# Kernel tuning notes

Measured on AMD Instinct MI355X. Metric: run time of the kernel, lower is better.

Reference implementation:

```python
import jax, jax.numpy as jnp
import numpy as np
import math

D_MODEL = 1024
NHEAD = 16
D_K = D_MODEL // NHEAD
NUM_LAYERS = 4
D_FF = 4096
SEQ = 2048
BATCH = 1
EPS = 1e-5


def _layer_norm(x, g, b):
    mu = jnp.mean(x, axis=-1, keepdims=True)
    var = jnp.mean((x - mu) ** 2, axis=-1, keepdims=True)
    return (x - mu) * jax.lax.rsqrt(var + EPS) * g + b


def setup_inputs() -> dict:
    key = jax.random.key(0)
    ks = jax.random.split(key, 16)
    s = 0.02
    L, D, F = NUM_LAYERS, D_MODEL, D_FF
    inp = {
        "x": jax.random.normal(ks[0], (BATCH, SEQ, D), dtype=jnp.float32),
        "wq": jax.random.normal(ks[1], (L, D, D), dtype=jnp.float32) * s,
        "bq": jnp.zeros((L, D), dtype=jnp.float32),
        "wk": jax.random.normal(ks[2], (L, D, D), dtype=jnp.float32) * s,
        "bk": jnp.zeros((L, D), dtype=jnp.float32),
        "wv": jax.random.normal(ks[3], (L, D, D), dtype=jnp.float32) * s,
        "bv": jnp.zeros((L, D), dtype=jnp.float32),
        "wo": jax.random.normal(ks[4], (L, D, D), dtype=jnp.float32) * s,
        "bo": jnp.zeros((L, D), dtype=jnp.float32),
        "w1": jax.random.normal(ks[5], (L, D, F), dtype=jnp.float32) * s,
        "b1": jnp.zeros((L, F), dtype=jnp.float32),
        "w2": jax.random.normal(ks[6], (L, F, D), dtype=jnp.float32) * s,
        "b2": jnp.zeros((L, D), dtype=jnp.float32),
        "ln1_g": jnp.ones((L, D), dtype=jnp.float32),
        "ln1_b": jnp.zeros((L, D), dtype=jnp.float32),
        "ln2_g": jnp.ones((L, D), dtype=jnp.float32),
        "ln2_b": jnp.zeros((L, D), dtype=jnp.float32),
    }
    return inp


def _transformer(x, wq, bq, wk, bk, wv, bv, wo, bo, w1, b1, w2, b2,
                 ln1_g, ln1_b, ln2_g, ln2_b):
    B, S, D = x.shape
    scale = math.sqrt(D_K)
    for l in range(NUM_LAYERS):
        # multi-head self-attention (manual QKV matmul + softmax + matmul)
        q = (x @ wq[l] + bq[l]).reshape(B, S, NHEAD, D_K).transpose(0, 2, 1, 3)
        k = (x @ wk[l] + bk[l]).reshape(B, S, NHEAD, D_K).transpose(0, 2, 1, 3)
        v = (x @ wv[l] + bv[l]).reshape(B, S, NHEAD, D_K).transpose(0, 2, 1, 3)
        scores = jnp.einsum('bhqd,bhkd->bhqk', q, k) / scale  # [B,H,S,S]
        attn = jax.nn.softmax(scores, axis=-1)
        ctx = jnp.einsum('bhqk,bhkd->bhqd', attn, v)
        ctx = ctx.transpose(0, 2, 1, 3).reshape(B, S, D)
        attn_out = ctx @ wo[l] + bo[l]
        x = _layer_norm(x + attn_out, ln1_g[l], ln1_b[l])
        # feed-forward network with gelu
        h = jax.nn.gelu(x @ w1[l] + b1[l])
        ffn_out = h @ w2[l] + b2[l]
        x = _layer_norm(x + ffn_out, ln2_g[l], ln2_b[l])
    return x


def reference(x, wq, bq, wk, bk, wv, bv, wo, bo, w1, b1, w2, b2,
              ln1_g, ln1_b, ln2_g, ln2_b):
    return _transformer(x, wq, bq, wk, bk, wv, bv, wo, bo, w1, b1, w2, b2,
                        ln1_g, ln1_b, ln2_g, ln2_b)
```

## Files before the change

### kernel.cpp

```cpp
#include <hip/hip_runtime.h>
#include <hip/hip_bf16.h>
#include <math.h>

typedef __hip_bfloat16 bf16;
typedef __attribute__((ext_vector_type(8))) short bf16x8;
typedef __attribute__((ext_vector_type(4))) short bf16x4;
typedef __attribute__((ext_vector_type(4))) float f32x4;

#define EPI_NONE 0
#define EPI_BIAS_BF16 1
#define EPI_BIAS_GELU_BF16 2

#define CLOG 0.18033688f

__device__ __forceinline__ void gload16(const void* g, void* l) {
  __builtin_amdgcn_global_load_lds((const __attribute__((address_space(1))) void*)g,
                                   (__attribute__((address_space(3))) void*)l, 16, 0, 0);
}

__device__ __forceinline__ float gelu_tanh(float x) {
  const float c = 0.7978845608028654f;
  float t = tanhf(c * (x + 0.044715f * x * x * x));
  return 0.5f * x * (1.0f + t);
}

__device__ __forceinline__ short bf16bits(float x) {
  bf16 h = __float2bfloat16(x);
  return *reinterpret_cast<const short*>(&h);
}

template<int BM, int BN, int BK, int EPI, typename CT>
__global__ __launch_bounds__(256) void gemm_bt(
    const bf16* __restrict__ A, long sAz, int lda,
    const bf16* __restrict__ Bt, long sBz, int ldb,
    CT* __restrict__ C, long sCz, int ldc,
    const float* __restrict__ bias,
    int K, float scale)
{
  constexpr int WM = BM / 2, WN = BN / 2;
  constexpr int MI = WM / 16, NJ = WN / 16;
  constexpr int NA = (BM * BK * 2) / 4096;
  constexpr int NB = (BN * BK * 2) / 4096;
  constexpr int ROWB = BK * 2;
  __shared__ __align__(16) bf16 As[BM * BK];
  __shared__ __align__(16) bf16 Bs[BN * BK];
  const int t = threadIdx.x;
  const int lane = t & 63, w = t >> 6;
  const int wm = (w >> 1) * WM, wn = (w & 1) * WN;
  const int quad = lane >> 4, r16 = lane & 15;
  const long z = blockIdx.z;
  const bf16* Ab = A + z * sAz + (long)blockIdx.y * BM * lda;
  const bf16* Bb = Bt + z * sBz + (long)blockIdx.x * BN * ldb;

  f32x4 acc[MI][NJ];
  #pragma unroll
  for (int i = 0; i < MI; ++i)
    #pragma unroll
    for (int j = 0; j < NJ; ++j)
      acc[i][j] = (f32x4){0.f, 0.f, 0.f, 0.f};

  for (int k0 = 0; k0 < K; k0 += BK) {
    __syncthreads();
    #pragma unroll
    for (int s = 0; s < NA; ++s) {
      int Lb = s * 4096 + t * 16;
      int row = Lb / ROWB, colb = Lb % ROWB;
      gload16((const char*)Ab + (long)row * (lda * 2) + k0 * 2 + colb, (char*)As + Lb);
    }
    #pragma unroll
    for (int s = 0; s < NB; ++s) {
      int Lb = s * 4096 + t * 16;
      int row = Lb / ROWB, colb = Lb % ROWB;
      gload16((const char*)Bb + (long)row * (ldb * 2) + k0 * 2 + colb, (char*)Bs + Lb);
    }
    __syncthreads();

    #pragma unroll
    for (int kk = 0; kk < BK / 32; ++kk) {
      bf16x8 af[MI], bfv[NJ];
      #pragma unroll
      for (int i = 0; i < MI; ++i)
        af[i] = *(const bf16x8*)&As[(wm + i * 16 + r16) * BK + kk * 32 + quad * 8];
      #pragma unroll
      for (int j = 0; j < NJ; ++j)
        bfv[j] = *(const bf16x8*)&Bs[(wn + j * 16 + r16) * BK + kk * 32 + quad * 8];
      #pragma unroll
      for (int i = 0; i < MI; ++i)
        #pragma unroll
        for (int j = 0; j < NJ; ++j)
          acc[i][j] = __builtin_amdgcn_mfma_f32_16x16x32_bf16(af[i], bfv[j], acc[i][j], 0, 0, 0);
    }
  }

  CT* Cb = C + z * sCz;
  #pragma unroll
  for (int i = 0; i < MI; ++i) {
    #pragma unroll
    for (int j = 0; j < NJ; ++j) {
      int col = blockIdx.x * BN + wn + j * 16 + r16;
      float bvv = 0.f;
      if constexpr (EPI == EPI_BIAS_BF16 || EPI == EPI_BIAS_GELU_BF16)
        bvv = bias[col];
      #pragma unroll
      for (int r = 0; r < 4; ++r) {
        long row = (long)blockIdx.y * BM + wm + i * 16 + quad * 4 + r;
        float val = acc[i][j][r] * scale + bvv;
        if constexpr (EPI == EPI_BIAS_GELU_BF16) val = gelu_tanh(val);
        if constexpr (sizeof(CT) == 2)
          Cb[row * (long)ldc + col] = __float2bfloat16(val);
        else
          Cb[row * (long)ldc + col] = val;
      }
    }
  }
}

__global__ __launch_bounds__(256) void flash_attn(
    const bf16* __restrict__ qkv, const bf16* __restrict__ vT,
    float* __restrict__ Osp, float2* __restrict__ ml)
{
  constexpr int SEQ = 2048, LDP = 72, LDPP = 80;
  __shared__ __align__(16) bf16 Qs[64 * 64];
  __shared__ __align__(16) bf16 Ks[64 * LDP];
  __shared__ __align__(16) bf16 VTs[64 * LDP];
  __shared__ __align__(16) bf16 Ps[64 * LDPP];

  const int t = threadIdx.x;
  const int lane = t & 63, w = t >> 6;
  const int quad = lane >> 4, r16 = lane & 15;
  const int wq0 = w * 16;
  const int s0 = blockIdx.x * 64;
  const int h = blockIdx.y;
  const int split = blockIdx.z;
  const int kt0 = split * 16, ktN = kt0 + 16;

  #pragma unroll
  for (int s = 0; s < 2; ++s) {
    int Lb = s * 4096 + t * 16;
    int row = Lb >> 7, colb = Lb & 127;
    int4 v = *(const int4*)(qkv + (long)(s0 + row) * 3072 + h * 64 + (colb >> 1));
    *(int4*)((char*)Qs + Lb) = v;
  }

  const bf16* kp[2]; const bf16* vp[2];
  int krow[2], kcolb[2];
  #pragma unroll
  for (int s = 0; s < 2; ++s) {
    int Lb = s * 4096 + t * 16;
    krow[s] = Lb >> 7; kcolb[s] = Lb & 127;
    kp[s] = qkv + 1024 + (long)h * 64 + (long)krow[s] * 3072 + (kcolb[s] >> 1);
    vp[s] = vT + (long)(h * 64 + krow[s]) * SEQ + (kcolb[s] >> 1);
  }

  int4 rk[2], rv[2];
  #pragma unroll
  for (int s = 0; s < 2; ++s) {
    rk[s] = *(const int4*)(kp[s] + (long)kt0 * 64 * 3072);
    rv[s] = *(const int4*)(vp[s] + (long)kt0 * 64);
  }

  __syncthreads();
  bf16x8 af_q[2];
  #pragma unroll
  for (int kk = 0; kk < 2; ++kk)
    af_q[kk] = *(const bf16x8*)&Qs[(wq0 + r16) * 64 + kk * 32 + quad * 8];

  f32x4 O[4];
  float m_s = -1e30f, l_s = 0.f;
  #pragma unroll
  for (int jd = 0; jd < 4; ++jd) O[jd] = (f32x4){0.f, 0.f, 0.f, 0.f};

  for (int kt = kt0; kt < ktN; ++kt) {
    __syncthreads();
    #pragma unroll
    for (int s = 0; s < 2; ++s) {
      *(int4*)((char*)Ks + (krow[s] * LDP * 2) + kcolb[s]) = rk[s];
      *(int4*)((char*)VTs + (krow[s] * LDP * 2) + kcolb[s]) = rv[s];
    }
    __syncthreads();

    if (kt + 1 < ktN) {
      long k0n = (long)(kt + 1) * 64;
      #pragma unroll
      for (int s = 0; s < 2; ++s) {
        rk[s] = *(const int4*)(kp[s] + k0n * 3072);
        rv[s] = *(const int4*)(vp[s] + k0n);
      }
    }

    f32x4 sc[4];
    #pragma unroll
    for (int j = 0; j < 4; ++j) sc[j] = (f32x4){0.f, 0.f, 0.f, 0.f};
    #pragma unroll
    for (int kk = 0; kk < 2; ++kk) {
      bf16x8 bk_f[4];
      #pragma unroll
      for (int j = 0; j < 4; ++j)
        bk_f[j] = *(const bf16x8*)&Ks[(j * 16 + r16) * LDP + kk * 32 + quad * 8];
      #pragma unroll
      for (int j = 0; j < 4; ++j)
        sc[j] = __builtin_amdgcn_mfma_f32_16x16x32_bf16(bk_f[j], af_q[kk], sc[j], 0, 0, 0);
    }

    float mj[4];
    #pragma unroll
    for (int j = 0; j < 4; ++j)
      mj[j] = fmaxf(fmaxf(sc[j][0], sc[j][1]), fmaxf(sc[j][2], sc[j][3]));
    float mx = fmaxf(fmaxf(mj[0], mj[1]), fmaxf(mj[2], mj[3]));
    mx = fmaxf(mx, __shfl_xor(mx, 16));
    mx = fmaxf(mx, __shfl_xor(mx, 32));
    float m_new = fmaxf(m_s, mx * CLOG);
    float alpha = exp2f(m_s - m_new);
    m_s = m_new;
    float p[4][4], sj[4];
    #pragma unroll
    for (int j = 0; j < 4; ++j) {
      #pragma unroll
      for (int r = 0; r < 4; ++r)
        p[j][r] = exp2f(fmaf(sc[j][r], CLOG, -m_new));
      sj[j] = (p[j][0] + p[j][1]) + (p[j][2] + p[j][3]);
    }
    float rs = (sj[0] + sj[1]) + (sj[2] + sj[3]);
    rs += __shfl_xor(rs, 16);
    rs += __shfl_xor(rs, 32);
    l_s = l_s * alpha + rs;

    float ar[4];
    #pragma unroll
    for (int r = 0; r < 4; ++r)
      ar[r] = __shfl(alpha, quad * 20 + r);
    #pragma unroll
    for (int jd = 0; jd < 4; ++jd)
      #pragma unroll
      for (int r = 0; r < 4; ++r)
        O[jd][r] *= ar[r];

    {
      bf16* pr = &Ps[(wq0 + r16) * LDPP + quad * 4];
      #pragma unroll
      for (int j = 0; j < 4; ++j) {
        bf16x4 pk;
        #pragma unroll
        for (int r = 0; r < 4; ++r)
          pk[r] = bf16bits(p[j][r]);
        *(bf16x4*)(pr + j * 16) = pk;
      }
    }

    #pragma unroll
    for (int kk = 0; kk < 2; ++kk) {
      bf16x8 af_p, bv_f[4];
      af_p = *(const bf16x8*)&Ps[(wq0 + r16) * LDPP + kk * 32 + quad * 8];
      #pragma unroll
      for (int jd = 0; jd < 4; ++jd)
        bv_f[jd] = *(const bf16x8*)&VTs[(jd * 16 + r16) * LDP + kk * 32 + quad * 8];
      #pragma unroll
      for (int jd = 0; jd < 4; ++jd)
        O[jd] = __builtin_amdgcn_mfma_f32_16x16x32_bf16(af_p, bv_f[jd], O[jd], 0, 0, 0);
    }
  }

  float* Ob = Osp + (long)split * SEQ * 1024;
  #pragma unroll
  for (int r = 0; r < 4; ++r) {
    long row = s0 + wq0 + quad * 4 + r;
    #pragma unroll
    for (int jd = 0; jd < 4; ++jd)
      Ob[row * 1024 + h * 64 + jd * 16 + r16] = O[jd][r];
  }
  if (quad == 0)
    ml[((long)(split * 16 + h)) * SEQ + (s0 + wq0 + r16)] = make_float2(m_s, l_s);
}

__global__ __launch_bounds__(256) void attn_combine(
    const float* __restrict__ Osp, const float2* __restrict__ ml,
    bf16* __restrict__ ctx)
{
  constexpr long SD = 2048L * 1024L;
  const int s = blockIdx.x;
  const int t = threadIdx.x;
  #pragma unroll
  for (int i = 0; i < 4; ++i) {
    int c = t + i * 256;
    int h = c >> 6;
    float2 a = ml[(long)h * 2048 + s];
    float2 b = ml[(long)(16 + h) * 2048 + s];
    float mC = fmaxf(a.x, b.x);
    float w0 = exp2f(a.x - mC), w1 = exp2f(b.x - mC);
    float inv = 1.f / (a.y * w0 + b.y * w1);
    float o = (Osp[(long)s * 1024 + c] * w0 + Osp[SD + (long)s * 1024 + c] * w1) * inv;
    ctx[(long)s * 1024 + c] = __float2bfloat16(o);
  }
}

__global__ __launch_bounds__(256) void transpose_cast(
    const float* __restrict__ in, bf16* __restrict__ out, int R, int C)
{
  __shared__ bf16 tile[32][33];
  const int tx = threadIdx.x, ty = threadIdx.y;
  const int r0 = blockIdx.y * 32, c0 = blockIdx.x * 32;
  #pragma unroll
  for (int d = 0; d < 32; d += 8)
    tile[ty + d][tx] = __float2bfloat16(in[(long)(r0 + ty + d) * C + c0 + tx]);
  __syncthreads();
  #pragma unroll
  for (int d = 0; d < 32; d += 8)
    out[(long)(c0 + ty + d) * R + r0 + tx] = tile[tx][ty + d];
}

__global__ __launch_bounds__(256) void transpose_cast3(
    const float* __restrict__ w0, const float* __restrict__ w1p,
    const float* __restrict__ w2p, bf16* __restrict__ out, int R, int C)
{
  __shared__ bf16 tile[32][33];
  const float* in = (blockIdx.z == 0) ? w0 : (blockIdx.z == 1) ? w1p : w2p;
  bf16* o = out + (long)blockIdx.z * R * C;
  const int tx = threadIdx.x, ty = threadIdx.y;
  const int r0 = blockIdx.y * 32, c0 = blockIdx.x * 32;
  #pragma unroll
  for (int d = 0; d < 32; d += 8)
    tile[ty + d][tx] = __float2bfloat16(in[(long)(r0 + ty + d) * C + c0 + tx]);
  __syncthreads();
  #pragma unroll
  for (int d = 0; d < 32; d += 8)
    o[(long)(c0 + ty + d) * R + r0 + tx] = tile[tx][ty + d];
}

__global__ __launch_bounds__(256) void transpose_bf16(
    const bf16* __restrict__ in, bf16* __restrict__ out, int R, int C, int ldin)
{
  __shared__ bf16 tile[32][33];
  const int tx = threadIdx.x, ty = threadIdx.y;
  const int r0 = blockIdx.y * 32, c0 = blockIdx.x * 32;
  #pragma unroll
  for (int d = 0; d < 32; d += 8)
    tile[ty + d][tx] = in[(long)(r0 + ty + d) * ldin + c0 + tx];
  __syncthreads();
  #pragma unroll
  for (int d = 0; d < 32; d += 8)
    out[(long)(c0 + ty + d) * R + r0 + tx] = tile[tx][ty + d];
}

__device__ __forceinline__ float blk_sum(float v, float* sh) {
  #pragma unroll
  for (int o = 32; o > 0; o >>= 1) v += __shfl_down(v, o);
  __syncthreads();
  if ((threadIdx.x & 63) == 0) sh[threadIdx.x >> 6] = v;
  __syncthreads();
  return sh[0] + sh[1] + sh[2] + sh[3];
}

__global__ __launch_bounds__(256) void ln_residual2(
    float* __restrict__ X, const float* __restrict__ d0, const float* __restrict__ d1,
    const float* __restrict__ bias,
    const float* __restrict__ g, const float* __restrict__ b,
    bf16* __restrict__ xb)
{
  __shared__ float sh[4];
  const int t = threadIdx.x;
  const long base = (long)blockIdx.x * 1024;
  float v[4]; float s = 0.f;
  #pragma unroll
  for (int i = 0; i < 4; ++i) {
    int c = t + i * 256;
    float val = X[base + c] + d0[base + c] + d1[base + c] + bias[c];
    v[i] = val; s += val;
  }
  s = blk_sum(s, sh);
  const float mu = s * (1.f / 1024.f);
  float s2 = 0.f;
  #pragma unroll
  for (int i = 0; i < 4; ++i) { float d = v[i] - mu; s2 += d * d; }
  s2 = blk_sum(s2, sh);
  const float rs = rsqrtf(s2 * (1.f / 1024.f) + 1e-5f);
  #pragma unroll
  for (int i = 0; i < 4; ++i) {
    int c = t + i * 256;
    float o = (v[i] - mu) * rs * g[c] + b[c];
    X[base + c] = o;
    xb[base + c] = __float2bfloat16(o);
  }
}

__global__ __launch_bounds__(256) void init_x(
    const float* __restrict__ xin, float* __restrict__ X, bf16* __restrict__ xb, int n)
{
  for (int i = blockIdx.x * 256 + threadIdx.x; i < n; i += gridDim.x * 256) {
    float v = xin[i];
    X[i] = v;
    xb[i] = __float2bfloat16(v);
  }
}

__global__ __launch_bounds__(256) void copy_out(
    const float* __restrict__ X, float* __restrict__ out, int n)
{
  for (int i = blockIdx.x * 256 + threadIdx.x; i < n; i += gridDim.x * 256)
    out[i] = X[i];
}

__global__ __launch_bounds__(256) void concat_bias(
    const float* __restrict__ bq, const float* __restrict__ bk,
    const float* __restrict__ bv, float* __restrict__ out, int n)
{
  for (int i = blockIdx.x * 256 + threadIdx.x; i < n; i += gridDim.x * 256) {
    int l = i / 3072, r = i % 3072;
    int j = r / 1024, c = r % 1024;
    const float* src = (j == 0) ? bq : (j == 1) ? bk : bv;
    out[i] = src[l * 1024 + c];
  }
}

extern "C" void kernel_launch(void* const* d_in, const int* in_sizes, int n_in,
                              void* d_out, int out_size, void* d_ws, size_t ws_size,
                              hipStream_t stream) {
  constexpr int S = 2048, D = 1024, F = 4096, L = 4;
  const float* xin = (const float*)d_in[0];
  const float* wq = (const float*)d_in[1];
  const float* bq = (const float*)d_in[2];
  const float* wk = (const float*)d_in[3];
  const float* bk = (const float*)d_in[4];
  const float* wv = (const float*)d_in[5];
  const float* bvp = (const float*)d_in[6];
  const float* wo = (const float*)d_in[7];
  const float* bo = (const float*)d_in[8];
  const float* w1 = (const float*)d_in[9];
  const float* b1 = (const float*)d_in[10];
  const float* w2 = (const float*)d_in[11];
  const float* b2 = (const float*)d_in[12];
  const float* ln1g = (const float*)d_in[13];
  const float* ln1b = (const float*)d_in[14];
  const float* ln2g = (const float*)d_in[15];
  const float* ln2b = (const float*)d_in[16];

  char* p = (char*)d_ws;
  float* X    = (float*)p; p += (long)S * D * 4;
  float* tmpf = (float*)p; p += 2L * S * D * 4;
  bf16* xb    = (bf16*)p;  p += (long)S * D * 2;
  bf16* qkv   = (bf16*)p;
  bf16* hb    = (bf16*)p;  p += (long)S * 3 * D * 2;
  bf16* ctx   = (bf16*)p;  p += (long)S * D * 2;
  bf16* vT    = (bf16*)p;  p += (long)S * D * 2;
  bf16* wT    = (bf16*)p;  p += (long)F * D * 2;
  float* bias3= (float*)p; p += (long)L * 3 * D * 4;
  float2* ml  = (float2*)p; p += 2L * 16 * S * 8;

  init_x<<<2048, 256, 0, stream>>>(xin, X, xb, S * D);
  concat_bias<<<48, 256, 0, stream>>>(bq, bk, bvp, bias3, L * 3 * D);

  for (int l = 0; l < L; ++l) {
    transpose_cast3<<<dim3(D / 32, D / 32, 3), dim3(32, 8), 0, stream>>>(
        wq + (long)l * D * D, wk + (long)l * D * D, wv + (long)l * D * D, wT, D, D);
    gemm_bt<128, 64, 64, EPI_BIAS_BF16, bf16><<<dim3(3 * D / 64, S / 128, 1), 256, 0, stream>>>(
        xb, 0L, D, wT, 0L, D, qkv, 0L, 3 * D, bias3 + l * 3 * D, D, 1.f);

    transpose_bf16<<<dim3(D / 32, S / 32), dim3(32, 8), 0, stream>>>(qkv + 2 * D, vT, S, D, 3 * D);

    flash_attn<<<dim3(S / 64, 16, 2), 256, 0, stream>>>(qkv, vT, tmpf, ml);
    attn_combine<<<S, 256, 0, stream>>>(tmpf, ml, ctx);

    transpose_cast<<<dim3(D / 32, D / 32), dim3(32, 8), 0, stream>>>(wo + (long)l * D * D, wT, D, D);
    gemm_bt<128, 64, 64, EPI_NONE, float><<<dim3(D / 64, S / 128, 2), 256, 0, stream>>>(
        ctx, (long)(D / 2), D, wT, (long)(D / 2), D, tmpf, (long)S * D, D, nullptr, D / 2, 1.f);
    ln_residual2<<<S, 256, 0, stream>>>(X, tmpf, tmpf + (long)S * D, bo + l * D,
                                        ln1g + l * D, ln1b + l * D, xb);

    transpose_cast<<<dim3(F / 32, D / 32), dim3(32, 8), 0, stream>>>(w1 + (long)l * D * F, wT, D, F);
    gemm_bt<128, 64, 64, EPI_BIAS_GELU_BF16, bf16><<<dim3(F / 64, S / 128, 1), 256, 0, stream>>>(
        xb, 0L, D, wT, 0L, D, hb, 0L, F, b1 + l * F, D, 1.f);
    transpose_cast<<<dim3(D / 32, F / 32), dim3(32, 8), 0, stream>>>(w2 + (long)l * F * D, wT, F, D);
    gemm_bt<128, 64, 64, EPI_NONE, float><<<dim3(D / 64, S / 128, 2), 256, 0, stream>>>(
        hb, (long)(F / 2), F, wT, (long)(F / 2), F, tmpf, (long)S * D, D, nullptr, F / 2, 1.f);
    ln_residual2<<<S, 256, 0, stream>>>(X, tmpf, tmpf + (long)S * D, b2 + l * D,
                                        ln2g + l * D, ln2b + l * D, xb);
  }
  copy_out<<<2048, 256, 0, stream>>>(X, (float*)d_out, S * D);
}
```

Baseline: 1.135 ms.

## Parameterize attention split count, load Q directly, widen FFN1 GEMM tile

```diff
diff --git a/kernel.cpp b/kernel.cpp
--- a/kernel.cpp
+++ b/kernel.cpp
@@ -117,10 +117,9 @@
 
 __global__ __launch_bounds__(256) void flash_attn(
     const bf16* __restrict__ qkv, const bf16* __restrict__ vT,
-    float* __restrict__ Osp, float2* __restrict__ ml)
+    float* __restrict__ Osp, float2* __restrict__ ml, int kts)
 {
   constexpr int SEQ = 2048, LDP = 72, LDPP = 80;
-  __shared__ __align__(16) bf16 Qs[64 * 64];
   __shared__ __align__(16) bf16 Ks[64 * LDP];
   __shared__ __align__(16) bf16 VTs[64 * LDP];
   __shared__ __align__(16) bf16 Ps[64 * LDPP];
@@ -132,14 +131,13 @@
   const int s0 = blockIdx.x * 64;
   const int h = blockIdx.y;
   const int split = blockIdx.z;
-  const int kt0 = split * 16, ktN = kt0 + 16;
-
-  #pragma unroll
-  for (int s = 0; s < 2; ++s) {
-    int Lb = s * 4096 + t * 16;
-    int row = Lb >> 7, colb = Lb & 127;
-    int4 v = *(const int4*)(qkv + (long)(s0 + row) * 3072 + h * 64 + (colb >> 1));
-    *(int4*)((char*)Qs + Lb) = v;
+  const int kt0 = split * kts, ktN = kt0 + kts;
+
+  bf16x8 af_q[2];
+  {
+    const bf16* qp = qkv + (long)(s0 + wq0 + r16) * 3072 + h * 64 + quad * 8;
+    af_q[0] = *(const bf16x8*)(qp);
+    af_q[1] = *(const bf16x8*)(qp + 32);
   }
 
   const bf16* kp[2]; const bf16* vp[2];
@@ -158,12 +156,6 @@
     rk[s] = *(const int4*)(kp[s] + (long)kt0 * 64 * 3072);
     rv[s] = *(const int4*)(vp[s] + (long)kt0 * 64);
   }
-
-  __syncthreads();
-  bf16x8 af_q[2];
-  #pragma unroll
-  for (int kk = 0; kk < 2; ++kk)
-    af_q[kk] = *(const bf16x8*)&Qs[(wq0 + r16) * 64 + kk * 32 + quad * 8];
 
   f32x4 O[4];
   float m_s = -1e30f, l_s = 0.f;
@@ -274,7 +266,7 @@
 
 __global__ __launch_bounds__(256) void attn_combine(
     const float* __restrict__ Osp, const float2* __restrict__ ml,
-    bf16* __restrict__ ctx)
+    bf16* __restrict__ ctx, int nsplit)
 {
   constexpr long SD = 2048L * 1024L;
   const int s = blockIdx.x;
@@ -283,13 +275,17 @@
   for (int i = 0; i < 4; ++i) {
     int c = t + i * 256;
     int h = c >> 6;
-    float2 a = ml[(long)h * 2048 + s];
-    float2 b = ml[(long)(16 + h) * 2048 + s];
-    float mC = fmaxf(a.x, b.x);
-    float w0 = exp2f(a.x - mC), w1 = exp2f(b.x - mC);
-    float inv = 1.f / (a.y * w0 + b.y * w1);
-    float o = (Osp[(long)s * 1024 + c] * w0 + Osp[SD + (long)s * 1024 + c] * w1) * inv;
-    ctx[(long)s * 1024 + c] = __float2bfloat16(o);
+    float mC = -1e30f;
+    for (int sp = 0; sp < nsplit; ++sp)
+      mC = fmaxf(mC, ml[(long)(sp * 16 + h) * 2048 + s].x);
+    float denom = 0.f, num = 0.f;
+    for (int sp = 0; sp < nsplit; ++sp) {
+      float2 a = ml[(long)(sp * 16 + h) * 2048 + s];
+      float wv = exp2f(a.x - mC);
+      denom += a.y * wv;
+      num += Osp[sp * SD + (long)s * 1024 + c] * wv;
+    }
+    ctx[(long)s * 1024 + c] = __float2bfloat16(num / denom);
   }
 }
 
@@ -433,9 +429,12 @@
   const float* ln2g = (const float*)d_in[15];
   const float* ln2b = (const float*)d_in[16];
 
+  const int nsplit = (ws_size >= 78u * 1024 * 1024) ? 4 : 2;
+  const int kts = 32 / nsplit;
+
   char* p = (char*)d_ws;
   float* X    = (float*)p; p += (long)S * D * 4;
-  float* tmpf = (float*)p; p += 2L * S * D * 4;
+  float* tmpf = (float*)p; p += (long)nsplit * S * D * 4;
   bf16* xb    = (bf16*)p;  p += (long)S * D * 2;
   bf16* qkv   = (bf16*)p;
   bf16* hb    = (bf16*)p;  p += (long)S * 3 * D * 2;
@@ -443,7 +442,7 @@
   bf16* vT    = (bf16*)p;  p += (long)S * D * 2;
   bf16* wT    = (bf16*)p;  p += (long)F * D * 2;
   float* bias3= (float*)p; p += (long)L * 3 * D * 4;
-  float2* ml  = (float2*)p; p += 2L * 16 * S * 8;
+  float2* ml  = (float2*)p; p += (long)nsplit * 16 * S * 8;
 
   init_x<<<2048, 256, 0, stream>>>(xin, X, xb, S * D);
   concat_bias<<<48, 256, 0, stream>>>(bq, bk, bvp, bias3, L * 3 * D);
@@ -456,8 +455,8 @@
 
     transpose_bf16<<<dim3(D / 32, S / 32), dim3(32, 8), 0, stream>>>(qkv + 2 * D, vT, S, D, 3 * D);
 
-    flash_attn<<<dim3(S / 64, 16, 2), 256, 0, stream>>>(qkv, vT, tmpf, ml);
-    attn_combine<<<S, 256, 0, stream>>>(tmpf, ml, ctx);
+    flash_attn<<<dim3(S / 64, 16, nsplit), 256, 0, stream>>>(qkv, vT, tmpf, ml, kts);
+    attn_combine<<<S, 256, 0, stream>>>(tmpf, ml, ctx, nsplit);
 
     transpose_cast<<<dim3(D / 32, D / 32), dim3(32, 8), 0, stream>>>(wo + (long)l * D * D, wT, D, D);
     gemm_bt<128, 64, 64, EPI_NONE, float><<<dim3(D / 64, S / 128, 2), 256, 0, stream>>>(
@@ -466,7 +465,7 @@
                                         ln1g + l * D, ln1b + l * D, xb);
 
     transpose_cast<<<dim3(F / 32, D / 32), dim3(32, 8), 0, stream>>>(w1 + (long)l * D * F, wT, D, F);
-    gemm_bt<128, 64, 64, EPI_BIAS_GELU_BF16, bf16><<<dim3(F / 64, S / 128, 1), 256, 0, stream>>>(
+    gemm_bt<128, 128, 64, EPI_BIAS_GELU_BF16, bf16><<<dim3(F / 128, S / 128, 1), 256, 0, stream>>>(
         xb, 0L, D, wT, 0L, D, hb, 0L, F, b1 + l * F, D, 1.f);
     transpose_cast<<<dim3(D / 32, F / 32), dim3(32, 8), 0, stream>>>(w2 + (long)l * F * D, wT, F, D);
     gemm_bt<128, 64, 64, EPI_NONE, float><<<dim3(D / 64, S / 128, 2), 256, 0, stream>>>(
```

New measurement: 1.175 ms. 1.04x slower.
